# Optimization experiments

Hardware: AMD Instinct MI355X
Metric: run time of the kernel (lower is better)

The kernel has to match this reference:

```python
import jax, jax.numpy as jnp
import numpy as np

B, T, D, H = 16, 2048, 512, 512  # batch, seq_len, input_dim, hidden_dim


def setup_inputs() -> dict:
    key = jax.random.key(0)
    k1, k2, k3 = jax.random.split(key, 3)
    x = jax.random.normal(k1, (B, T, D), dtype=jnp.float32)
    # vanilla tanh RnnCell parameters
    W_xh = jax.random.normal(k2, (D, H), dtype=jnp.float32) / np.float32(np.sqrt(D))
    W_hh = jax.random.normal(k3, (H, H), dtype=jnp.float32) / np.float32(np.sqrt(H))
    b = jnp.zeros((H,), dtype=jnp.float32)
    # DFA feedback matrix, 'diagonal' init branch: diag(linspace(0,1,H))
    A = jnp.diag(jnp.linspace(0.0, 1.0, H).astype(jnp.float32))
    return {"x": x, "W_xh": W_xh, "W_hh": W_hh, "b": b, "A": A}


def reference(x, W_xh, W_hh, b, A):
    # Forward of DfaRnn: sequential RNN loop. detach() does not change forward
    # values, so this is a plain tanh RNN scan. A only affects the backward.
    Bb = x.shape[0]
    h0 = jnp.zeros((Bb, W_hh.shape[0]), dtype=x.dtype)

    def step(h, xt):
        h_new = jnp.tanh(xt @ W_xh + h @ W_hh + b)
        return h_new, h_new

    _, hs = jax.lax.scan(step, h0, jnp.swapaxes(x, 0, 1))  # [T,B,H]
    return jnp.swapaxes(hs, 0, 1)  # [B,T,H]
```

## Files before the change

kernel.cpp:

```cpp
#include <hip/hip_runtime.h>
#include <cmath>

#define B_ 16
#define T_ 2048
#define D_ 512
#define H_ 512

__global__ __launch_bounds__(256) void gemm_xw(
    const float* __restrict__ x,
    const float* __restrict__ Wxh,
    const float* __restrict__ bias,
    float* __restrict__ out)
{
    const int tid = threadIdx.x;
    const int n0 = blockIdx.x * 128;
    const int m0 = blockIdx.y * 128;

    __shared__ float As[8][132];
    __shared__ float Bs[8][132];

    const int tx = tid & 15, ty = tid >> 4;
    float acc[8][8] = {};

    const int arow = tid >> 1;
    const int akq  = (tid & 1) * 4;
    const int brow = tid >> 5;
    const int bcol = (tid & 31) * 4;

    for (int k0 = 0; k0 < D_; k0 += 8) {
        float4 a4 = *(const float4*)(x + (size_t)(m0 + arow) * D_ + k0 + akq);
        float4 b4 = *(const float4*)(Wxh + (size_t)(k0 + brow) * H_ + n0 + bcol);
        __syncthreads();
        As[akq + 0][arow] = a4.x;
        As[akq + 1][arow] = a4.y;
        As[akq + 2][arow] = a4.z;
        As[akq + 3][arow] = a4.w;
        *(float4*)(&Bs[brow][bcol]) = b4;
        __syncthreads();
#pragma unroll
        for (int kk = 0; kk < 8; ++kk) {
            float4 a0 = *(const float4*)(&As[kk][ty * 8]);
            float4 a1 = *(const float4*)(&As[kk][ty * 8 + 4]);
            float4 b0 = *(const float4*)(&Bs[kk][tx * 8]);
            float4 b1 = *(const float4*)(&Bs[kk][tx * 8 + 4]);
            float a_[8] = {a0.x, a0.y, a0.z, a0.w, a1.x, a1.y, a1.z, a1.w};
            float b_[8] = {b0.x, b0.y, b0.z, b0.w, b1.x, b1.y, b1.z, b1.w};
#pragma unroll
            for (int i = 0; i < 8; ++i)
#pragma unroll
                for (int j = 0; j < 8; ++j) acc[i][j] += a_[i] * b_[j];
        }
    }

    const float4 bv0 = *(const float4*)(bias + n0 + tx * 8);
    const float4 bv1 = *(const float4*)(bias + n0 + tx * 8 + 4);
    const float bb[8] = {bv0.x, bv0.y, bv0.z, bv0.w, bv1.x, bv1.y, bv1.z, bv1.w};
#pragma unroll
    for (int i = 0; i < 8; ++i) {
        const int m = m0 + ty * 8 + i;
        float4 o0, o1;
        o0.x = acc[i][0] + bb[0]; o0.y = acc[i][1] + bb[1];
        o0.z = acc[i][2] + bb[2]; o0.w = acc[i][3] + bb[3];
        o1.x = acc[i][4] + bb[4]; o1.y = acc[i][5] + bb[5];
        o1.z = acc[i][6] + bb[6]; o1.w = acc[i][7] + bb[7];
        *(float4*)(out + (size_t)m * H_ + n0 + tx * 8)     = o0;
        *(float4*)(out + (size_t)m * H_ + n0 + tx * 8 + 4) = o1;
    }
}

__device__ __forceinline__ void bar_lds() {
    asm volatile("s_waitcnt lgkmcnt(0)\n\ts_barrier" ::: "memory");
}

__global__ __launch_bounds__(512, 2) void rnn_rec(
    const float* __restrict__ Whh,
    float* __restrict__ out,
    unsigned long long* __restrict__ ws)
{
    const int tid = threadIdx.x;
    const int b = blockIdx.x & 15;
    const int s = blockIdx.x >> 4;
    const int w = tid >> 6;
    const int l = tid & 63;
    const int g = l >> 3;
    const int cl = l & 7;
    const int c_glob = (s << 6) + (w << 3) + cl;
    const int grot = g << 3;

    __shared__ float h_lds[2][H_];

    float W_reg[64];
    {
#pragma unroll
        for (int r = 0; r < 64; ++r) {
            const int row = (g << 6) + ((grot + r) & 63);
            const float* addr = Whh + (size_t)row * H_ + c_glob;
            asm volatile("global_load_dword %0, %1, off"
                         : "=v"(W_reg[r]) : "v"(addr));
        }
        asm volatile("s_waitcnt vmcnt(0)" ::: "memory");
    }

    h_lds[0][tid] = 0.0f;
    __syncthreads();

    float* outb = out + (size_t)b * T_ * H_;
    unsigned long long* wsb = ws + (size_t)b * 2 * H_;

    const int c_pref = (s << 6) + (w << 3) + l;
    float xw0 = 0.0f, xw1 = 0.0f, xw2 = 0.0f;
    if (l < 8) {
        xw0 = outb[(size_t)0 * H_ + c_pref];
        xw1 = outb[(size_t)1 * H_ + c_pref];
        xw2 = outb[(size_t)2 * H_ + c_pref];
    }

    const int q = (w < 7) ? (w + (w >= s ? 1 : 0)) : -1;

    for (int t = 0; t < T_; ++t) {
        const float* hb = h_lds[t & 1];
        float acc = 0.0f;
#pragma unroll
        for (int i = 0; i < 16; ++i) {
            const int idx = (g << 6) + ((grot + (i << 2)) & 63);
            const float4 h4 = *(const float4*)(hb + idx);
            acc += h4.x * W_reg[4 * i + 0] + h4.y * W_reg[4 * i + 1]
                 + h4.z * W_reg[4 * i + 2] + h4.w * W_reg[4 * i + 3];
        }
        acc += __shfl_xor(acc, 8);
        acc += __shfl_xor(acc, 16);
        acc += __shfl_xor(acc, 32);

        const unsigned int tag = (unsigned int)(t + 1);
        const int slot = (t + 1) & 1;
        unsigned long long* wslot = wsb + (size_t)slot * H_;
        float* hn = h_lds[(t + 1) & 1];

        if (l < 8) {
            union { unsigned int u; float f; } cv;
            cv.f = tanhf(acc + xw0);
            unsigned long long pv =
                ((unsigned long long)tag << 32) | (unsigned long long)cv.u;
            __hip_atomic_store(wslot + c_pref, pv, __ATOMIC_RELAXED,
                               __HIP_MEMORY_SCOPE_AGENT);
            outb[(size_t)t * H_ + c_pref] = cv.f;
            hn[c_pref] = cv.f;
            xw0 = xw1;
            xw1 = xw2;
            xw2 = (t + 3 < T_) ? outb[(size_t)(t + 3) * H_ + c_pref] : 0.0f;
        }

        if (q >= 0) {
            unsigned long long* src = wslot + (q << 6) + l;
            unsigned long long v;
            do {
                v = __hip_atomic_load(src, __ATOMIC_RELAXED,
                                      __HIP_MEMORY_SCOPE_AGENT);
            } while ((unsigned int)(v >> 32) < tag);
            union { unsigned int u; float f; } cv2;
            cv2.u = (unsigned int)v;
            hn[(q << 6) + l] = cv2.f;
        }

        bar_lds();
    }
}

extern "C" void kernel_launch(void* const* d_in, const int* in_sizes, int n_in,
                              void* d_out, int out_size, void* d_ws,
                              size_t ws_size, hipStream_t stream) {
    const float* x    = (const float*)d_in[0];
    const float* Wxh  = (const float*)d_in[1];
    const float* Whh  = (const float*)d_in[2];
    const float* bias = (const float*)d_in[3];
    float* out = (float*)d_out;

    hipMemsetAsync(d_ws, 0, (size_t)B_ * 2 * H_ * sizeof(unsigned long long),
                   stream);

    dim3 ggrid(H_ / 128, (B_ * T_) / 128, 1);
    gemm_xw<<<ggrid, 256, 0, stream>>>(x, Wxh, bias, out);

    rnn_rec<<<128, 512, 0, stream>>>(Whh, out, (unsigned long long*)d_ws);
}
```

Before: 2.896 ms.

## Have each wavefront poll the full hidden state directly, dropping block barriers

Each wavefront now reads the whole tagged hidden vector for the step from the global workspace with vector loads, spinning until all tags match. The data goes into a per-wave LDS staging area instead of a block-shared buffer. This removes the per-step block-wide barrier and the split where some waves fetched remote slices while others computed. In exchange every wave issues many more global loads per step, all polling the same cache lines, which adds L2 traffic and contention.

Measured after the change: 5.364 ms. 1.85x slower.

```diff
diff --git a/kernel.cpp b/kernel.cpp
--- a/kernel.cpp
+++ b/kernel.cpp
@@ -5,6 +5,8 @@
 #define T_ 2048
 #define D_ 512
 #define H_ 512
+
+typedef __attribute__((ext_vector_type(4))) unsigned int uint4v;
 
 __global__ __launch_bounds__(256) void gemm_xw(
     const float* __restrict__ x,
@@ -66,10 +68,6 @@
         *(float4*)(out + (size_t)m * H_ + n0 + tx * 8)     = o0;
         *(float4*)(out + (size_t)m * H_ + n0 + tx * 8 + 4) = o1;
     }
-}
-
-__device__ __forceinline__ void bar_lds() {
-    asm volatile("s_waitcnt lgkmcnt(0)\n\ts_barrier" ::: "memory");
 }
 
 __global__ __launch_bounds__(512, 2) void rnn_rec(
@@ -84,85 +82,109 @@
     const int l = tid & 63;
     const int g = l >> 3;
     const int cl = l & 7;
-    const int c_glob = (s << 6) + (w << 3) + cl;
-    const int grot = g << 3;
-
-    __shared__ float h_lds[2][H_];
+    const int c = (s << 6) + (w << 3) + cl;
+
+    __shared__ float hstage[8][8 * 72];
+    float* myst = hstage[w];
 
     float W_reg[64];
     {
+        const float* wbase = Whh + (size_t)(g << 6) * H_ + c;
 #pragma unroll
         for (int r = 0; r < 64; ++r) {
-            const int row = (g << 6) + ((grot + r) & 63);
-            const float* addr = Whh + (size_t)row * H_ + c_glob;
+            const float* addr = wbase + (size_t)r * H_;
             asm volatile("global_load_dword %0, %1, off"
                          : "=v"(W_reg[r]) : "v"(addr));
         }
         asm volatile("s_waitcnt vmcnt(0)" ::: "memory");
     }
 
-    h_lds[0][tid] = 0.0f;
-    __syncthreads();
-
     float* outb = out + (size_t)b * T_ * H_;
     unsigned long long* wsb = ws + (size_t)b * 2 * H_;
 
-    const int c_pref = (s << 6) + (w << 3) + l;
     float xw0 = 0.0f, xw1 = 0.0f, xw2 = 0.0f;
     if (l < 8) {
-        xw0 = outb[(size_t)0 * H_ + c_pref];
-        xw1 = outb[(size_t)1 * H_ + c_pref];
-        xw2 = outb[(size_t)2 * H_ + c_pref];
-    }
-
-    const int q = (w < 7) ? (w + (w >= s ? 1 : 0)) : -1;
+        xw0 = outb[(size_t)0 * H_ + c];
+        xw1 = outb[(size_t)1 * H_ + c];
+        xw2 = outb[(size_t)2 * H_ + c];
+    }
 
     for (int t = 0; t < T_; ++t) {
-        const float* hb = h_lds[t & 1];
         float acc = 0.0f;
-#pragma unroll
-        for (int i = 0; i < 16; ++i) {
-            const int idx = (g << 6) + ((grot + (i << 2)) & 63);
-            const float4 h4 = *(const float4*)(hb + idx);
-            acc += h4.x * W_reg[4 * i + 0] + h4.y * W_reg[4 * i + 1]
-                 + h4.z * W_reg[4 * i + 2] + h4.w * W_reg[4 * i + 3];
+        if (t > 0) {
+            const unsigned int tn = (unsigned int)t;
+            const unsigned long long* src =
+                wsb + (size_t)(t & 1) * H_ + (g << 6) + (cl << 3);
+            uint4v c0, c1, c2, c3;
+            asm volatile("global_load_dwordx4 %0, %1, off sc0 sc1"
+                         : "=v"(c0) : "v"(src));
+            asm volatile("global_load_dwordx4 %0, %1, off offset:16 sc0 sc1"
+                         : "=v"(c1) : "v"(src));
+            asm volatile("global_load_dwordx4 %0, %1, off offset:32 sc0 sc1"
+                         : "=v"(c2) : "v"(src));
+            asm volatile("global_load_dwordx4 %0, %1, off offset:48 sc0 sc1"
+                         : "=v"(c3) : "v"(src));
+            for (;;) {
+                asm volatile("s_waitcnt vmcnt(0)"
+                             : "+v"(c0), "+v"(c1), "+v"(c2), "+v"(c3)
+                             :: "memory");
+                __builtin_amdgcn_sched_barrier(0);
+                const bool ok0 = (c0.y >= tn) & (c0.w >= tn);
+                const bool ok1 = (c1.y >= tn) & (c1.w >= tn);
+                const bool ok2 = (c2.y >= tn) & (c2.w >= tn);
+                const bool ok3 = (c3.y >= tn) & (c3.w >= tn);
+                if (__all(ok0 & ok1 & ok2 & ok3)) break;
+                if (!ok0)
+                    asm volatile("global_load_dwordx4 %0, %1, off sc0 sc1"
+                                 : "=v"(c0) : "v"(src));
+                if (!ok1)
+                    asm volatile(
+                        "global_load_dwordx4 %0, %1, off offset:16 sc0 sc1"
+                        : "=v"(c1) : "v"(src));
+                if (!ok2)
+                    asm volatile(
+                        "global_load_dwordx4 %0, %1, off offset:32 sc0 sc1"
+                        : "=v"(c2) : "v"(src));
+                if (!ok3)
+                    asm volatile(
+                        "global_load_dwordx4 %0, %1, off offset:48 sc0 sc1"
+                        : "=v"(c3) : "v"(src));
+            }
+            float4 f0, f1;
+            f0.x = __uint_as_float(c0.x); f0.y = __uint_as_float(c0.z);
+            f0.z = __uint_as_float(c1.x); f0.w = __uint_as_float(c1.z);
+            f1.x = __uint_as_float(c2.x); f1.y = __uint_as_float(c2.z);
+            f1.z = __uint_as_float(c3.x); f1.w = __uint_as_float(c3.z);
+            *(float4*)(myst + g * 72 + (cl << 3))     = f0;
+            *(float4*)(myst + g * 72 + (cl << 3) + 4) = f1;
+            asm volatile("s_waitcnt lgkmcnt(0)" ::: "memory");
+            __builtin_amdgcn_sched_barrier(0);
+            const float4* hb = (const float4*)(myst + g * 72);
+#pragma unroll
+            for (int i = 0; i < 16; ++i) {
+                const float4 h4 = hb[i];
+                acc += h4.x * W_reg[4 * i + 0] + h4.y * W_reg[4 * i + 1]
+                     + h4.z * W_reg[4 * i + 2] + h4.w * W_reg[4 * i + 3];
+            }
         }
         acc += __shfl_xor(acc, 8);
         acc += __shfl_xor(acc, 16);
         acc += __shfl_xor(acc, 32);
 
-        const unsigned int tag = (unsigned int)(t + 1);
-        const int slot = (t + 1) & 1;
-        unsigned long long* wslot = wsb + (size_t)slot * H_;
-        float* hn = h_lds[(t + 1) & 1];
-
+        const unsigned int tagp = (unsigned int)(t + 1);
+        unsigned long long* wpub = wsb + (size_t)((t + 1) & 1) * H_;
         if (l < 8) {
             union { unsigned int u; float f; } cv;
             cv.f = tanhf(acc + xw0);
             unsigned long long pv =
-                ((unsigned long long)tag << 32) | (unsigned long long)cv.u;
-            __hip_atomic_store(wslot + c_pref, pv, __ATOMIC_RELAXED,
+                ((unsigned long long)tagp << 32) | (unsigned long long)cv.u;
+            __hip_atomic_store(wpub + c, pv, __ATOMIC_RELAXED,
                                __HIP_MEMORY_SCOPE_AGENT);
-            outb[(size_t)t * H_ + c_pref] = cv.f;
-            hn[c_pref] = cv.f;
+            outb[(size_t)t * H_ + c] = cv.f;
             xw0 = xw1;
             xw1 = xw2;
-            xw2 = (t + 3 < T_) ? outb[(size_t)(t + 3) * H_ + c_pref] : 0.0f;
-        }
-
-        if (q >= 0) {
-            unsigned long long* src = wslot + (q << 6) + l;
-            unsigned long long v;
-            do {
-                v = __hip_atomic_load(src, __ATOMIC_RELAXED,
-                                      __HIP_MEMORY_SCOPE_AGENT);
-            } while ((unsigned int)(v >> 32) < tag);
-            union { unsigned int u; float f; } cv2;
-            cv2.u = (unsigned int)v;
-            hn[(q << 6) + l] = cv2.f;
-        }
-
-        bar_lds();
+            xw2 = (t + 3 < T_) ? outb[(size_t)(t + 3) * H_ + c] : 0.0f;
+        }
     }
 }
 
```

## Fuse input projection GEMM into recurrent kernel with register-resident W_xh

Applied to the files above, without the earlier changes.

Removes the separate x@W_xh GEMM kernel and computes each timestep's input projection inside the recurrent kernel. W_xh is held in registers alongside W_hh, and x rows are prefetched into a small LDS ring buffer. The projection for step t+1 is computed between publishing h_t and spinning on other blocks' results, so it can hide in the sync latency. The cost is double the register footprint per thread (128 weight registers) and extra work on the sequential critical path.

Measured after the change: 3.256 ms. 1.12x slower.

```diff
diff --git a/kernel.cpp b/kernel.cpp
--- a/kernel.cpp
+++ b/kernel.cpp
@@ -6,74 +6,31 @@
 #define D_ 512
 #define H_ 512
 
-__global__ __launch_bounds__(256) void gemm_xw(
-    const float* __restrict__ x,
-    const float* __restrict__ Wxh,
-    const float* __restrict__ bias,
-    float* __restrict__ out)
-{
-    const int tid = threadIdx.x;
-    const int n0 = blockIdx.x * 128;
-    const int m0 = blockIdx.y * 128;
-
-    __shared__ float As[8][132];
-    __shared__ float Bs[8][132];
-
-    const int tx = tid & 15, ty = tid >> 4;
-    float acc[8][8] = {};
-
-    const int arow = tid >> 1;
-    const int akq  = (tid & 1) * 4;
-    const int brow = tid >> 5;
-    const int bcol = (tid & 31) * 4;
-
-    for (int k0 = 0; k0 < D_; k0 += 8) {
-        float4 a4 = *(const float4*)(x + (size_t)(m0 + arow) * D_ + k0 + akq);
-        float4 b4 = *(const float4*)(Wxh + (size_t)(k0 + brow) * H_ + n0 + bcol);
-        __syncthreads();
-        As[akq + 0][arow] = a4.x;
-        As[akq + 1][arow] = a4.y;
-        As[akq + 2][arow] = a4.z;
-        As[akq + 3][arow] = a4.w;
-        *(float4*)(&Bs[brow][bcol]) = b4;
-        __syncthreads();
-#pragma unroll
-        for (int kk = 0; kk < 8; ++kk) {
-            float4 a0 = *(const float4*)(&As[kk][ty * 8]);
-            float4 a1 = *(const float4*)(&As[kk][ty * 8 + 4]);
-            float4 b0 = *(const float4*)(&Bs[kk][tx * 8]);
-            float4 b1 = *(const float4*)(&Bs[kk][tx * 8 + 4]);
-            float a_[8] = {a0.x, a0.y, a0.z, a0.w, a1.x, a1.y, a1.z, a1.w};
-            float b_[8] = {b0.x, b0.y, b0.z, b0.w, b1.x, b1.y, b1.z, b1.w};
-#pragma unroll
-            for (int i = 0; i < 8; ++i)
-#pragma unroll
-                for (int j = 0; j < 8; ++j) acc[i][j] += a_[i] * b_[j];
-        }
-    }
-
-    const float4 bv0 = *(const float4*)(bias + n0 + tx * 8);
-    const float4 bv1 = *(const float4*)(bias + n0 + tx * 8 + 4);
-    const float bb[8] = {bv0.x, bv0.y, bv0.z, bv0.w, bv1.x, bv1.y, bv1.z, bv1.w};
-#pragma unroll
-    for (int i = 0; i < 8; ++i) {
-        const int m = m0 + ty * 8 + i;
-        float4 o0, o1;
-        o0.x = acc[i][0] + bb[0]; o0.y = acc[i][1] + bb[1];
-        o0.z = acc[i][2] + bb[2]; o0.w = acc[i][3] + bb[3];
-        o1.x = acc[i][4] + bb[4]; o1.y = acc[i][5] + bb[5];
-        o1.z = acc[i][6] + bb[6]; o1.w = acc[i][7] + bb[7];
-        *(float4*)(out + (size_t)m * H_ + n0 + tx * 8)     = o0;
-        *(float4*)(out + (size_t)m * H_ + n0 + tx * 8 + 4) = o1;
-    }
-}
-
 __device__ __forceinline__ void bar_lds() {
     asm volatile("s_waitcnt lgkmcnt(0)\n\ts_barrier" ::: "memory");
 }
 
-__global__ __launch_bounds__(512, 2) void rnn_rec(
+#define SLICE_DOT(RES, XR, REG)                                              \
+    {                                                                        \
+        float a_ = 0.0f;                                                     \
+        _Pragma("unroll")                                                    \
+        for (int i_ = 0; i_ < 16; ++i_) {                                    \
+            const int idx_ = (g << 6) + ((grot + (i_ << 2)) & 63);           \
+            const float4 v4_ = *(const float4*)((XR) + idx_);                \
+            a_ += v4_.x * (REG)[4 * i_ + 0] + v4_.y * (REG)[4 * i_ + 1]      \
+                + v4_.z * (REG)[4 * i_ + 2] + v4_.w * (REG)[4 * i_ + 3];     \
+        }                                                                    \
+        a_ += __shfl_xor(a_, 8);                                             \
+        a_ += __shfl_xor(a_, 16);                                            \
+        a_ += __shfl_xor(a_, 32);                                            \
+        (RES) = a_;                                                          \
+    }
+
+__global__ __launch_bounds__(512, 2) void rnn_fused(
+    const float* __restrict__ x,
+    const float* __restrict__ Wxh,
     const float* __restrict__ Whh,
+    const float* __restrict__ bias,
     float* __restrict__ out,
     unsigned long long* __restrict__ ws)
 {
@@ -84,70 +41,88 @@
     const int l = tid & 63;
     const int g = l >> 3;
     const int cl = l & 7;
-    const int c_glob = (s << 6) + (w << 3) + cl;
+    const int c = (s << 6) + (w << 3) + cl;
     const int grot = g << 3;
 
     __shared__ float h_lds[2][H_];
+    __shared__ float xring[4][D_];
 
     float W_reg[64];
+    float X_reg[64];
     {
 #pragma unroll
         for (int r = 0; r < 64; ++r) {
             const int row = (g << 6) + ((grot + r) & 63);
-            const float* addr = Whh + (size_t)row * H_ + c_glob;
+            const float* addr = Whh + (size_t)row * H_ + c;
             asm volatile("global_load_dword %0, %1, off"
                          : "=v"(W_reg[r]) : "v"(addr));
+        }
+#pragma unroll
+        for (int r = 0; r < 64; ++r) {
+            const int row = (g << 6) + ((grot + r) & 63);
+            const float* addr = Wxh + (size_t)row * H_ + c;
+            asm volatile("global_load_dword %0, %1, off"
+                         : "=v"(X_reg[r]) : "v"(addr));
         }
         asm volatile("s_waitcnt vmcnt(0)" ::: "memory");
     }
 
+    const float* xb = x + (size_t)b * T_ * D_;
+    float* outb = out + (size_t)b * T_ * H_;
+    unsigned long long* wsb = ws + (size_t)b * 2 * H_;
+    const float bias_c = bias[c];
+
+    if (tid < 128) {
+#pragma unroll
+        for (int r = 0; r < 3; ++r) {
+            float4 v = *(const float4*)(xb + (size_t)r * D_ + tid * 4);
+            *(float4*)(&xring[r][tid * 4]) = v;
+        }
+    }
+    float4 xrow_hold = {0.f, 0.f, 0.f, 0.f};
+    if (tid < 128)
+        xrow_hold = *(const float4*)(xb + (size_t)3 * D_ + tid * 4);
+
     h_lds[0][tid] = 0.0f;
     __syncthreads();
 
-    float* outb = out + (size_t)b * T_ * H_;
-    unsigned long long* wsb = ws + (size_t)b * 2 * H_;
-
-    const int c_pref = (s << 6) + (w << 3) + l;
-    float xw0 = 0.0f, xw1 = 0.0f, xw2 = 0.0f;
-    if (l < 8) {
-        xw0 = outb[(size_t)0 * H_ + c_pref];
-        xw1 = outb[(size_t)1 * H_ + c_pref];
-        xw2 = outb[(size_t)2 * H_ + c_pref];
-    }
+    float xw_hold;
+    SLICE_DOT(xw_hold, xring[0], X_reg);
+    xw_hold += bias_c;
 
     const int q = (w < 7) ? (w + (w >= s ? 1 : 0)) : -1;
 
     for (int t = 0; t < T_; ++t) {
-        const float* hb = h_lds[t & 1];
-        float acc = 0.0f;
-#pragma unroll
-        for (int i = 0; i < 16; ++i) {
-            const int idx = (g << 6) + ((grot + (i << 2)) & 63);
-            const float4 h4 = *(const float4*)(hb + idx);
-            acc += h4.x * W_reg[4 * i + 0] + h4.y * W_reg[4 * i + 1]
-                 + h4.z * W_reg[4 * i + 2] + h4.w * W_reg[4 * i + 3];
+        if (tid < 128) {
+            if (t + 3 < T_)
+                *(float4*)(&xring[(t + 3) & 3][tid * 4]) = xrow_hold;
+            if (t + 4 < T_)
+                xrow_hold =
+                    *(const float4*)(xb + (size_t)(t + 4) * D_ + tid * 4);
         }
-        acc += __shfl_xor(acc, 8);
-        acc += __shfl_xor(acc, 16);
-        acc += __shfl_xor(acc, 32);
+
+        float acc;
+        SLICE_DOT(acc, h_lds[t & 1], W_reg);
 
         const unsigned int tag = (unsigned int)(t + 1);
-        const int slot = (t + 1) & 1;
-        unsigned long long* wslot = wsb + (size_t)slot * H_;
+        unsigned long long* wslot = wsb + (size_t)((t + 1) & 1) * H_;
         float* hn = h_lds[(t + 1) & 1];
 
         if (l < 8) {
             union { unsigned int u; float f; } cv;
-            cv.f = tanhf(acc + xw0);
+            cv.f = tanhf(acc + xw_hold);
             unsigned long long pv =
                 ((unsigned long long)tag << 32) | (unsigned long long)cv.u;
-            __hip_atomic_store(wslot + c_pref, pv, __ATOMIC_RELAXED,
+            __hip_atomic_store(wslot + c, pv, __ATOMIC_RELAXED,
                                __HIP_MEMORY_SCOPE_AGENT);
-            outb[(size_t)t * H_ + c_pref] = cv.f;
-            hn[c_pref] = cv.f;
-            xw0 = xw1;
-            xw1 = xw2;
-            xw2 = (t + 3 < T_) ? outb[(size_t)(t + 3) * H_ + c_pref] : 0.0f;
+            outb[(size_t)t * H_ + c] = cv.f;
+            hn[c] = cv.f;
+        }
+
+        if (t + 1 < T_) {
+            float a;
+            SLICE_DOT(a, xring[(t + 1) & 3], X_reg);
+            xw_hold = a + bias_c;
         }
 
         if (q >= 0) {
@@ -178,8 +153,6 @@
     hipMemsetAsync(d_ws, 0, (size_t)B_ * 2 * H_ * sizeof(unsigned long long),
                    stream);
 
-    dim3 ggrid(H_ / 128, (B_ * T_) / 128, 1);
-    gemm_xw<<<ggrid, 256, 0, stream>>>(x, Wxh, bias, out);
-
-    rnn_rec<<<128, 512, 0, stream>>>(Whh, out, (unsigned long long*)d_ws);
+    rnn_fused<<<128, 512, 0, stream>>>(x, Wxh, Whh, bias, out,
+                                       (unsigned long long*)d_ws);
 }
```
